# Kernel tuning notes

Measured on AMD Instinct MI355X. Metric: run time of the kernel, lower is better.

The kernel has to match this reference:

```python
import jax, jax.numpy as jnp
import numpy as np

ANGLE = 0.5  # angular margin from init_kwargs


def setup_inputs() -> dict:
    key = jax.random.key(0)
    k1, k2, k3 = jax.random.split(key, 3)
    B, F, C = 512, 128, 100000
    # scale by 0.1 so exp(features @ w) and exp(modulus * cos) stay finite in fp32
    features = jax.random.normal(k1, (B, F), dtype=jnp.float32) * 0.1
    w = jax.random.normal(k2, (F, C), dtype=jnp.float32) * 0.1
    target = jax.random.randint(k3, (B,), 0, C, dtype=jnp.int64)
    return {"features": features, "w": w, "target": target}


def reference(features, w, target):
    B = features.shape[0]
    rows = jnp.arange(B)
    # norms: [B,1] and [1,C]
    features_modulus = jnp.sqrt(jnp.sum(features ** 2, axis=1, keepdims=True))
    w_modulus = jnp.sqrt(jnp.sum(w ** 2, axis=0, keepdims=True))
    modulus = features_modulus * w_modulus  # [B, C]
    logits = jnp.matmul(features, w)  # [B, C] (computed once; torch computes it twice)
    cos_theta = logits / modulus / 1.01
    theta = jnp.arccos(cos_theta) + ANGLE
    cos_theta_plus = jnp.cos(theta)
    margin_logits = modulus * cos_theta_plus  # [B, C]
    top = jnp.exp(margin_logits[rows, target])  # [B]
    down_ = jnp.exp(logits)  # [B, C]
    down = jnp.sum(down_, axis=1) - down_[rows, target] + top  # [B]
    return -jnp.sum(jnp.log(top / down)) / B
```

## Files before the change

kernel.cpp:

```cpp
#include <hip/hip_runtime.h>

#define F_DIM   128
#define C_DIM   100000
#define B_ROWS  512
#define ANGLE   0.5f
#define CPB     128
#define NCB     782
#define OOB_PAD 96.0f
#define LOG2E   1.4426950408889634f
#define GRID_MAIN 512

typedef __attribute__((ext_vector_type(4))) float        f32x4;
typedef __attribute__((ext_vector_type(8))) short        bf16x8;
typedef __attribute__((ext_vector_type(4))) unsigned int u32x4;

static __device__ __forceinline__ unsigned int pk2(float a, float b) {
    unsigned int r;
    asm("v_cvt_pk_bf16_f32 %0, %1, %2" : "=v"(r) : "v"(a), "v"(b));
    return r;
}

__global__ __launch_bounds__(512, 4)
void arc_main(const float* __restrict__ feat,
              const float* __restrict__ w,
              float* __restrict__ pp)
{
    __shared__ unsigned short lBt[128 * 128];

    const int tid  = threadIdx.x;
    const int bid  = blockIdx.x;
    const int lane = tid & 63;
    const int wv   = tid >> 6;
    const int quad = lane >> 4;
    const int l15  = lane & 15;

    #pragma unroll 1
    for (int cbi = 0; cbi < 2; ++cbi) {
        const int cb = bid + cbi * GRID_MAIN;
        if (cb >= NCB) break;
        const int c0 = cb * CPB;
        if (cbi) __syncthreads();

        {
            const int cq = tid & 31;
            const int ko = tid >> 5;
            const int gc = c0 + cq * 4;
            f32x4 wr[8];
            if (gc < C_DIM) {
                const float* wp = w + (size_t)ko * 8 * C_DIM + gc;
                #pragma unroll
                for (int i = 0; i < 8; ++i)
                    wr[i] = *(const f32x4*)(wp + (size_t)i * C_DIM);
            } else {
                #pragma unroll
                for (int i = 0; i < 8; ++i)
                    wr[i] = (f32x4){0.f, 0.f, 0.f, 0.f};
            }
            #pragma unroll
            for (int j = 0; j < 4; ++j) {
                const int cls = cq * 4 + j;
                union { u32x4 u; bf16x8 h; } c;
                c.u[0] = pk2(wr[0][j] * LOG2E, wr[1][j] * LOG2E);
                c.u[1] = pk2(wr[2][j] * LOG2E, wr[3][j] * LOG2E);
                c.u[2] = pk2(wr[4][j] * LOG2E, wr[5][j] * LOG2E);
                c.u[3] = pk2(wr[6][j] * LOG2E, wr[7][j] * LOG2E);
                const int f = (cls & 12) | ((cls ^ (cls >> 4)) & 3);
                *(bf16x8*)&lBt[cls * 128 + ((ko ^ f) << 3)] = c.h;
            }
        }
        __syncthreads();

        #pragma unroll 1
        for (int half = 0; half < 2; ++half) {
            const int r0 = half << 8;

            bf16x8 fB[2][4];
            #pragma unroll
            for (int s = 0; s < 2; ++s) {
                const int b = r0 + wv * 32 + s * 16 + l15;
                #pragma unroll
                for (int ks = 0; ks < 4; ++ks) {
                    const int k0 = ks * 32 + quad * 8;
                    const f32x4 u0 = *(const f32x4*)(feat + b * F_DIM + k0);
                    const f32x4 u1 = *(const f32x4*)(feat + b * F_DIM + k0 + 4);
                    union { u32x4 u; bf16x8 h; } c;
                    c.u[0] = pk2(u0[0], u0[1]); c.u[1] = pk2(u0[2], u0[3]);
                    c.u[2] = pk2(u1[0], u1[1]); c.u[3] = pk2(u1[2], u1[3]);
                    fB[s][ks] = c.h;
                }
            }

            float eA0 = 0.f, eA1 = 0.f, eA2 = 0.f, eA3 = 0.f;
            float eB0 = 0.f, eB1 = 0.f, eB2 = 0.f, eB3 = 0.f;
            #pragma unroll
            for (int m = 0; m < 8; ++m) {
                f32x4 a0 = {0.f, 0.f, 0.f, 0.f};
                f32x4 a1 = {0.f, 0.f, 0.f, 0.f};
                const int rb = (m * 16 + l15) * 128;
                const int fr = (l15 & 12) | ((l15 ^ m) & 3);
                #pragma unroll
                for (int ks = 0; ks < 4; ++ks) {
                    const int pc = (ks * 4 + quad) ^ fr;
                    const bf16x8 af = *(const bf16x8*)&lBt[rb + (pc << 3)];
                    a0 = __builtin_amdgcn_mfma_f32_16x16x32_bf16(af, fB[0][ks], a0, 0, 0, 0);
                    a1 = __builtin_amdgcn_mfma_f32_16x16x32_bf16(af, fB[1][ks], a1, 0, 0, 0);
                }
                eA0 += __builtin_amdgcn_exp2f(a0[0]); eA1 += __builtin_amdgcn_exp2f(a0[1]);
                eA2 += __builtin_amdgcn_exp2f(a0[2]); eA3 += __builtin_amdgcn_exp2f(a0[3]);
                eB0 += __builtin_amdgcn_exp2f(a1[0]); eB1 += __builtin_amdgcn_exp2f(a1[1]);
                eB2 += __builtin_amdgcn_exp2f(a1[2]); eB3 += __builtin_amdgcn_exp2f(a1[3]);
            }

            float esum0 = (eA0 + eA1) + (eA2 + eA3);
            float esum1 = (eB0 + eB1) + (eB2 + eB3);
            esum0 += __shfl_xor(esum0, 16); esum0 += __shfl_xor(esum0, 32);
            esum1 += __shfl_xor(esum1, 16); esum1 += __shfl_xor(esum1, 32);
            if (lane < 16) {
                const int r = r0 + wv * 32 + lane;
                pp[(size_t)cb * 512 + r]      = esum0;
                pp[(size_t)cb * 512 + r + 16] = esum1;
            }
        }
    }
}

__global__ void arc_row(const float* __restrict__ feat,
                        const float* __restrict__ w,
                        const int*   __restrict__ target,
                        const float* __restrict__ pp,
                        float* __restrict__ term)
{
    const int b    = blockIdx.x;
    const int lane = threadIdx.x;
    const int t    = target[b];

    float dot = 0.f, wsq = 0.f, fsq = 0.f, rs = 0.f;
    #pragma unroll
    for (int h = 0; h < 2; ++h) {
        const int f   = lane + h * 64;
        const float fv = feat[b * F_DIM + f];
        const float wc = w[(size_t)f * C_DIM + t];
        dot += fv * wc;
        wsq += wc * wc;
        fsq += fv * fv;
    }
    #pragma unroll
    for (int j = 0; j < 13; ++j) {
        const int c = lane + j * 64;
        if (c < NCB) rs += pp[(size_t)c * 512 + b];
    }

    #pragma unroll
    for (int off = 32; off > 0; off >>= 1) {
        dot += __shfl_xor(dot, off);
        wsq += __shfl_xor(wsq, off);
        fsq += __shfl_xor(fsq, off);
        rs  += __shfl_xor(rs,  off);
    }
    if (lane == 0) {
        const float mod = sqrtf(fsq) * sqrtf(wsq);
        float ct = dot / (mod * 1.01f);
        ct = fminf(1.f, fmaxf(-1.f, ct));
        const float th   = acosf(ct) + ANGLE;
        const float marg = mod * cosf(th);
        const float down = rs - OOB_PAD - expf(dot) + expf(marg);
        term[b] = marg - logf(down);
    }
}

__global__ void arc_loss(const float* __restrict__ term,
                         float* __restrict__ out)
{
    __shared__ float red[B_ROWS];
    const int b = threadIdx.x;
    red[b] = term[b];
    __syncthreads();
    #pragma unroll
    for (int st = 256; st > 0; st >>= 1) {
        if (b < st) red[b] += red[b + st];
        __syncthreads();
    }
    if (b == 0) out[0] = -red[0] / (float)B_ROWS;
}

extern "C" void kernel_launch(void* const* d_in, const int* in_sizes, int n_in,
                              void* d_out, int out_size, void* d_ws, size_t ws_size,
                              hipStream_t stream)
{
    const float* feat   = (const float*)d_in[0];
    const float* w      = (const float*)d_in[1];
    const int*   target = (const int*)d_in[2];

    float* pp   = (float*)d_ws;
    float* term = pp + (size_t)NCB * 512;

    arc_main<<<dim3(GRID_MAIN), 512, 0, stream>>>(feat, w, pp);
    arc_row<<<B_ROWS, 64, 0, stream>>>(feat, w, target, pp, term);
    arc_loss<<<1, B_ROWS, 0, stream>>>(term, (float*)d_out);
}
```

Measured before the change: 129.9 us.

## Fuse row finalization and loss reduction into main kernel via atomics and last-block

Merges the three launches into a memset plus one kernel. Per-row exp sums are accumulated with atomicAdd into a 512-entry rowsum instead of a per-block partial array, and each block computes the target-class margin terms for the targets that fall in its class tiles. The last block to finish, detected with an atomic counter, does the final log and mean reduction. Both weight tiles are also prefetched into registers up front to overlap the second tile's global load with the first tile's compute. The cost is extra atomics, serialized per-target work inside blocks, and much higher register pressure from holding two weight tiles.

Result: slower. 197.4 us (+52.0%).

```diff
diff --git a/kernel.cpp b/kernel.cpp
--- a/kernel.cpp
+++ b/kernel.cpp
@@ -20,12 +20,129 @@
     return r;
 }
 
+static __device__ __forceinline__ void stage_write(unsigned short* lBt,
+                                                   const f32x4* wr,
+                                                   int cq, int ko)
+{
+    #pragma unroll
+    for (int j = 0; j < 4; ++j) {
+        const int cls = cq * 4 + j;
+        union { u32x4 u; bf16x8 h; } c;
+        c.u[0] = pk2(wr[0][j] * LOG2E, wr[1][j] * LOG2E);
+        c.u[1] = pk2(wr[2][j] * LOG2E, wr[3][j] * LOG2E);
+        c.u[2] = pk2(wr[4][j] * LOG2E, wr[5][j] * LOG2E);
+        c.u[3] = pk2(wr[6][j] * LOG2E, wr[7][j] * LOG2E);
+        const int f = (cls & 12) | ((cls ^ (cls >> 4)) & 3);
+        *(bf16x8*)&lBt[cls * 128 + ((ko ^ f) << 3)] = c.h;
+    }
+}
+
+static __device__ __forceinline__ void compute_cb(const unsigned short* lBt,
+                                                  const float* __restrict__ feat,
+                                                  float* __restrict__ rowsum,
+                                                  int wv, int lane, int quad, int l15)
+{
+    #pragma unroll 1
+    for (int half = 0; half < 2; ++half) {
+        const int r0 = half << 8;
+
+        bf16x8 fB[2][4];
+        #pragma unroll
+        for (int s = 0; s < 2; ++s) {
+            const int b = r0 + wv * 32 + s * 16 + l15;
+            #pragma unroll
+            for (int ks = 0; ks < 4; ++ks) {
+                const int k0 = ks * 32 + quad * 8;
+                const f32x4 u0 = *(const f32x4*)(feat + b * F_DIM + k0);
+                const f32x4 u1 = *(const f32x4*)(feat + b * F_DIM + k0 + 4);
+                union { u32x4 u; bf16x8 h; } c;
+                c.u[0] = pk2(u0[0], u0[1]); c.u[1] = pk2(u0[2], u0[3]);
+                c.u[2] = pk2(u1[0], u1[1]); c.u[3] = pk2(u1[2], u1[3]);
+                fB[s][ks] = c.h;
+            }
+        }
+
+        float eA0 = 0.f, eA1 = 0.f, eA2 = 0.f, eA3 = 0.f;
+        float eB0 = 0.f, eB1 = 0.f, eB2 = 0.f, eB3 = 0.f;
+        #pragma unroll
+        for (int m = 0; m < 8; ++m) {
+            f32x4 a0 = {0.f, 0.f, 0.f, 0.f};
+            f32x4 a1 = {0.f, 0.f, 0.f, 0.f};
+            const int rb = (m * 16 + l15) * 128;
+            const int fr = (l15 & 12) | ((l15 ^ m) & 3);
+            #pragma unroll
+            for (int ks = 0; ks < 4; ++ks) {
+                const int pc = (ks * 4 + quad) ^ fr;
+                const bf16x8 af = *(const bf16x8*)&lBt[rb + (pc << 3)];
+                a0 = __builtin_amdgcn_mfma_f32_16x16x32_bf16(af, fB[0][ks], a0, 0, 0, 0);
+                a1 = __builtin_amdgcn_mfma_f32_16x16x32_bf16(af, fB[1][ks], a1, 0, 0, 0);
+            }
+            eA0 += __builtin_amdgcn_exp2f(a0[0]); eA1 += __builtin_amdgcn_exp2f(a0[1]);
+            eA2 += __builtin_amdgcn_exp2f(a0[2]); eA3 += __builtin_amdgcn_exp2f(a0[3]);
+            eB0 += __builtin_amdgcn_exp2f(a1[0]); eB1 += __builtin_amdgcn_exp2f(a1[1]);
+            eB2 += __builtin_amdgcn_exp2f(a1[2]); eB3 += __builtin_amdgcn_exp2f(a1[3]);
+        }
+
+        float esum0 = (eA0 + eA1) + (eA2 + eA3);
+        float esum1 = (eB0 + eB1) + (eB2 + eB3);
+        esum0 += __shfl_xor(esum0, 16); esum0 += __shfl_xor(esum0, 32);
+        esum1 += __shfl_xor(esum1, 16); esum1 += __shfl_xor(esum1, 32);
+        if (lane < 16) {
+            const int r = r0 + wv * 32 + lane;
+            atomicAdd(&rowsum[r],      esum0);
+            atomicAdd(&rowsum[r + 16], esum1);
+        }
+    }
+}
+
+static __device__ __forceinline__ void do_targets(const float* __restrict__ feat,
+                                                  const float* __restrict__ w,
+                                                  float* __restrict__ margv,
+                                                  float* __restrict__ expdot,
+                                                  int c0, int tgt, int wv, int lane)
+{
+    unsigned long long mask = __ballot((unsigned)(tgt - c0) < CPB);
+    while (mask) {
+        const int src = (int)__ffsll(mask) - 1;
+        mask &= mask - 1;
+        const int row = wv * 64 + src;
+        const int tb  = __shfl(tgt, src);
+        const float f1 = feat[row * F_DIM + lane];
+        const float f2 = feat[row * F_DIM + lane + 64];
+        const float w1 = w[(size_t)lane * C_DIM + tb];
+        const float w2 = w[(size_t)(lane + 64) * C_DIM + tb];
+        float dot = fmaf(f1, w1, f2 * w2);
+        float wsq = fmaf(w1, w1, w2 * w2);
+        float fsq = fmaf(f1, f1, f2 * f2);
+        #pragma unroll
+        for (int off = 32; off > 0; off >>= 1) {
+            dot += __shfl_xor(dot, off);
+            wsq += __shfl_xor(wsq, off);
+            fsq += __shfl_xor(fsq, off);
+        }
+        if (lane == src) {
+            const float mod = sqrtf(fsq) * sqrtf(wsq);
+            float ct = dot / (mod * 1.01f);
+            ct = fminf(1.f, fmaxf(-1.f, ct));
+            const float th = acosf(ct) + ANGLE;
+            margv[row]  = mod * cosf(th);
+            expdot[row] = expf(dot);
+        }
+    }
+}
+
 __global__ __launch_bounds__(512, 4)
 void arc_main(const float* __restrict__ feat,
               const float* __restrict__ w,
-              float* __restrict__ pp)
+              const int*   __restrict__ target,
+              float* __restrict__ rowsum,
+              float* __restrict__ margv,
+              float* __restrict__ expdot,
+              unsigned int* __restrict__ cnt,
+              float* __restrict__ out)
 {
     __shared__ unsigned short lBt[128 * 128];
+    __shared__ unsigned int   sOld;
 
     const int tid  = threadIdx.x;
     const int bid  = blockIdx.x;
@@ -33,154 +150,67 @@
     const int wv   = tid >> 6;
     const int quad = lane >> 4;
     const int l15  = lane & 15;
-
-    #pragma unroll 1
-    for (int cbi = 0; cbi < 2; ++cbi) {
-        const int cb = bid + cbi * GRID_MAIN;
-        if (cb >= NCB) break;
-        const int c0 = cb * CPB;
-        if (cbi) __syncthreads();
-
-        {
-            const int cq = tid & 31;
-            const int ko = tid >> 5;
-            const int gc = c0 + cq * 4;
-            f32x4 wr[8];
-            if (gc < C_DIM) {
-                const float* wp = w + (size_t)ko * 8 * C_DIM + gc;
-                #pragma unroll
-                for (int i = 0; i < 8; ++i)
-                    wr[i] = *(const f32x4*)(wp + (size_t)i * C_DIM);
-            } else {
-                #pragma unroll
-                for (int i = 0; i < 8; ++i)
-                    wr[i] = (f32x4){0.f, 0.f, 0.f, 0.f};
-            }
-            #pragma unroll
-            for (int j = 0; j < 4; ++j) {
-                const int cls = cq * 4 + j;
-                union { u32x4 u; bf16x8 h; } c;
-                c.u[0] = pk2(wr[0][j] * LOG2E, wr[1][j] * LOG2E);
-                c.u[1] = pk2(wr[2][j] * LOG2E, wr[3][j] * LOG2E);
-                c.u[2] = pk2(wr[4][j] * LOG2E, wr[5][j] * LOG2E);
-                c.u[3] = pk2(wr[6][j] * LOG2E, wr[7][j] * LOG2E);
-                const int f = (cls & 12) | ((cls ^ (cls >> 4)) & 3);
-                *(bf16x8*)&lBt[cls * 128 + ((ko ^ f) << 3)] = c.h;
-            }
-        }
+    const int tgt  = target[tid];
+
+    const int  cb0  = bid;
+    const int  cb1  = bid + GRID_MAIN;
+    const bool has2 = (cb1 < NCB);
+
+    const int cq = tid & 31;
+    const int ko = tid >> 5;
+    f32x4 wr[8], wr2[8];
+    {
+        const float* wp = w + (size_t)ko * 8 * C_DIM + (cb0 * CPB + cq * 4);
+        #pragma unroll
+        for (int i = 0; i < 8; ++i)
+            wr[i] = *(const f32x4*)(wp + (size_t)i * C_DIM);
+    }
+    if (has2) {
+        const int gc = cb1 * CPB + cq * 4;
+        if (gc < C_DIM) {
+            const float* wp = w + (size_t)ko * 8 * C_DIM + gc;
+            #pragma unroll
+            for (int i = 0; i < 8; ++i)
+                wr2[i] = *(const f32x4*)(wp + (size_t)i * C_DIM);
+        } else {
+            #pragma unroll
+            for (int i = 0; i < 8; ++i)
+                wr2[i] = (f32x4){0.f, 0.f, 0.f, 0.f};
+        }
+    }
+
+    stage_write(lBt, wr, cq, ko);
+    __syncthreads();
+    compute_cb(lBt, feat, rowsum, wv, lane, quad, l15);
+    do_targets(feat, w, margv, expdot, cb0 * CPB, tgt, wv, lane);
+
+    if (has2) {
         __syncthreads();
-
-        #pragma unroll 1
-        for (int half = 0; half < 2; ++half) {
-            const int r0 = half << 8;
-
-            bf16x8 fB[2][4];
-            #pragma unroll
-            for (int s = 0; s < 2; ++s) {
-                const int b = r0 + wv * 32 + s * 16 + l15;
-                #pragma unroll
-                for (int ks = 0; ks < 4; ++ks) {
-                    const int k0 = ks * 32 + quad * 8;
-                    const f32x4 u0 = *(const f32x4*)(feat + b * F_DIM + k0);
-                    const f32x4 u1 = *(const f32x4*)(feat + b * F_DIM + k0 + 4);
-                    union { u32x4 u; bf16x8 h; } c;
-                    c.u[0] = pk2(u0[0], u0[1]); c.u[1] = pk2(u0[2], u0[3]);
-                    c.u[2] = pk2(u1[0], u1[1]); c.u[3] = pk2(u1[2], u1[3]);
-                    fB[s][ks] = c.h;
-                }
-            }
-
-            float eA0 = 0.f, eA1 = 0.f, eA2 = 0.f, eA3 = 0.f;
-            float eB0 = 0.f, eB1 = 0.f, eB2 = 0.f, eB3 = 0.f;
-            #pragma unroll
-            for (int m = 0; m < 8; ++m) {
-                f32x4 a0 = {0.f, 0.f, 0.f, 0.f};
-                f32x4 a1 = {0.f, 0.f, 0.f, 0.f};
-                const int rb = (m * 16 + l15) * 128;
-                const int fr = (l15 & 12) | ((l15 ^ m) & 3);
-                #pragma unroll
-                for (int ks = 0; ks < 4; ++ks) {
-                    const int pc = (ks * 4 + quad) ^ fr;
-                    const bf16x8 af = *(const bf16x8*)&lBt[rb + (pc << 3)];
-                    a0 = __builtin_amdgcn_mfma_f32_16x16x32_bf16(af, fB[0][ks], a0, 0, 0, 0);
-                    a1 = __builtin_amdgcn_mfma_f32_16x16x32_bf16(af, fB[1][ks], a1, 0, 0, 0);
-                }
-                eA0 += __builtin_amdgcn_exp2f(a0[0]); eA1 += __builtin_amdgcn_exp2f(a0[1]);
-                eA2 += __builtin_amdgcn_exp2f(a0[2]); eA3 += __builtin_amdgcn_exp2f(a0[3]);
-                eB0 += __builtin_amdgcn_exp2f(a1[0]); eB1 += __builtin_amdgcn_exp2f(a1[1]);
-                eB2 += __builtin_amdgcn_exp2f(a1[2]); eB3 += __builtin_amdgcn_exp2f(a1[3]);
-            }
-
-            float esum0 = (eA0 + eA1) + (eA2 + eA3);
-            float esum1 = (eB0 + eB1) + (eB2 + eB3);
-            esum0 += __shfl_xor(esum0, 16); esum0 += __shfl_xor(esum0, 32);
-            esum1 += __shfl_xor(esum1, 16); esum1 += __shfl_xor(esum1, 32);
-            if (lane < 16) {
-                const int r = r0 + wv * 32 + lane;
-                pp[(size_t)cb * 512 + r]      = esum0;
-                pp[(size_t)cb * 512 + r + 16] = esum1;
-            }
-        }
-    }
-}
-
-__global__ void arc_row(const float* __restrict__ feat,
-                        const float* __restrict__ w,
-                        const int*   __restrict__ target,
-                        const float* __restrict__ pp,
-                        float* __restrict__ term)
-{
-    const int b    = blockIdx.x;
-    const int lane = threadIdx.x;
-    const int t    = target[b];
-
-    float dot = 0.f, wsq = 0.f, fsq = 0.f, rs = 0.f;
-    #pragma unroll
-    for (int h = 0; h < 2; ++h) {
-        const int f   = lane + h * 64;
-        const float fv = feat[b * F_DIM + f];
-        const float wc = w[(size_t)f * C_DIM + t];
-        dot += fv * wc;
-        wsq += wc * wc;
-        fsq += fv * fv;
-    }
-    #pragma unroll
-    for (int j = 0; j < 13; ++j) {
-        const int c = lane + j * 64;
-        if (c < NCB) rs += pp[(size_t)c * 512 + b];
-    }
-
-    #pragma unroll
-    for (int off = 32; off > 0; off >>= 1) {
-        dot += __shfl_xor(dot, off);
-        wsq += __shfl_xor(wsq, off);
-        fsq += __shfl_xor(fsq, off);
-        rs  += __shfl_xor(rs,  off);
-    }
-    if (lane == 0) {
-        const float mod = sqrtf(fsq) * sqrtf(wsq);
-        float ct = dot / (mod * 1.01f);
-        ct = fminf(1.f, fmaxf(-1.f, ct));
-        const float th   = acosf(ct) + ANGLE;
-        const float marg = mod * cosf(th);
-        const float down = rs - OOB_PAD - expf(dot) + expf(marg);
-        term[b] = marg - logf(down);
-    }
-}
-
-__global__ void arc_loss(const float* __restrict__ term,
-                         float* __restrict__ out)
-{
-    __shared__ float red[B_ROWS];
-    const int b = threadIdx.x;
-    red[b] = term[b];
+        stage_write(lBt, wr2, cq, ko);
+        __syncthreads();
+        compute_cb(lBt, feat, rowsum, wv, lane, quad, l15);
+        do_targets(feat, w, margv, expdot, cb1 * CPB, tgt, wv, lane);
+    }
+
+    __threadfence();
     __syncthreads();
-    #pragma unroll
-    for (int st = 256; st > 0; st >>= 1) {
-        if (b < st) red[b] += red[b + st];
+    if (tid == 0) sOld = atomicAdd(cnt, 1u);
+    __syncthreads();
+    if (sOld == GRID_MAIN - 1) {
+        __threadfence();
+        float* red = (float*)lBt;
+        const float m  = margv[tid];
+        const float rs = rowsum[tid];
+        const float dn = rs - OOB_PAD - expdot[tid] + expf(m);
+        red[tid] = m - logf(dn);
         __syncthreads();
-    }
-    if (b == 0) out[0] = -red[0] / (float)B_ROWS;
+        #pragma unroll
+        for (int st = 256; st > 0; st >>= 1) {
+            if (tid < st) red[tid] += red[tid + st];
+            __syncthreads();
+        }
+        if (tid == 0) out[0] = -red[0] / (float)B_ROWS;
+    }
 }
 
 extern "C" void kernel_launch(void* const* d_in, const int* in_sizes, int n_in,
@@ -191,10 +221,13 @@
     const float* w      = (const float*)d_in[1];
     const int*   target = (const int*)d_in[2];
 
-    float* pp   = (float*)d_ws;
-    float* term = pp + (size_t)NCB * 512;
-
-    arc_main<<<dim3(GRID_MAIN), 512, 0, stream>>>(feat, w, pp);
-    arc_row<<<B_ROWS, 64, 0, stream>>>(feat, w, target, pp, term);
-    arc_loss<<<1, B_ROWS, 0, stream>>>(term, (float*)d_out);
-}
+    float*        rowsum = (float*)d_ws;
+    unsigned int* cnt    = (unsigned int*)(rowsum + B_ROWS);
+    float*        margv  = (float*)(cnt + 1);
+    float*        expdot = margv + B_ROWS;
+
+    hipMemsetAsync(d_ws, 0, (B_ROWS + 1) * sizeof(float), stream);
+    arc_main<<<dim3(GRID_MAIN), 512, 0, stream>>>(feat, w, target,
+                                                  rowsum, margv, expdot,
+                                                  cnt, (float*)d_out);
+}
```
